# Kernel tuning notes

Hardware: AMD Instinct MI355X
Metric: run time of the kernel (lower is better)

## Reference

```python
import jax, jax.numpy as jnp
import numpy as np

B, D, F_IN, F_OUT = 4, 4096, 128, 128
LEAKY_SLOPE = 0.2


def setup_inputs() -> dict:
    key = jax.random.key(0)
    k_x, k_adj, k_W, k_as, k_at = jax.random.split(key, 5)
    x = jax.random.normal(k_x, (B, D, F_IN), dtype=jnp.float32)
    adj = jax.random.randint(k_adj, (B, D, D), 0, 2, dtype=jnp.int32)
    # xavier-uniform-like init for params
    lim_W = float(np.sqrt(6.0 / (F_IN + F_OUT)))
    W = jax.random.uniform(k_W, (F_IN, F_OUT), minval=-lim_W, maxval=lim_W, dtype=jnp.float32)
    lim_a = float(np.sqrt(6.0 / (F_OUT + 1)))
    a_src = jax.random.uniform(k_as, (F_OUT, 1), minval=-lim_a, maxval=lim_a, dtype=jnp.float32)
    a_tgt = jax.random.uniform(k_at, (F_OUT, 1), minval=-lim_a, maxval=lim_a, dtype=jnp.float32)
    bias = jnp.zeros((F_OUT,), dtype=jnp.float32)
    return {"x": x, "adj": adj, "W": W, "a_src": a_src, "a_tgt": a_tgt, "bias": bias}


def reference(x, adj, W, a_src, a_tgt, bias):
    # x: [B, D, F_in], adj: [B, D, D] (0/1), W: [F_in, F_out]
    Wh = x @ W  # [B, D, F_out]
    f_src = (Wh @ a_src)[..., 0]  # [B, D]
    f_tgt = (Wh @ a_tgt)[..., 0]  # [B, D]
    # additive attention: e_ij = LeakyReLU(f_src_i + f_tgt_j)
    e = jax.nn.leaky_relu(f_src[:, :, None] + f_tgt[:, None, :], negative_slope=LEAKY_SLOPE)  # [B, D, D]
    # torch code masked_fills with -inf then replaces inf with 0 -> masked scores become 0
    e = jnp.where(adj == 0, jnp.zeros((), e.dtype), e)
    attn = jax.nn.softmax(e, axis=-1)  # [B, D, D]
    attn = jnp.clip(attn, 0.0, 1.0)
    h_prime = jnp.einsum('bij,bjf->bif', attn, Wh) + bias  # [B, D, F_out]
    return h_prime, attn
```

## Files before the change

kernel.cpp:

```cpp
#include <hip/hip_runtime.h>

#define BB 4
#define DD 4096
#define FF 128
#define SLOPE 0.2f

typedef float f32x4 __attribute__((ext_vector_type(4)));
typedef int   i32x4 __attribute__((ext_vector_type(4)));
typedef short bf16x8 __attribute__((ext_vector_type(8)));

#define SOFT_BARRIER() do { \
  asm volatile("s_waitcnt lgkmcnt(0)" ::: "memory"); \
  __builtin_amdgcn_s_barrier(); \
} while (0)

__device__ __forceinline__ unsigned short f2bf(float v) {
  union { float f; unsigned u; } c; c.f = v;
  unsigned r = c.u + 0x7FFFu + ((c.u >> 16) & 1u);
  return (unsigned short)(r >> 16);
}

__global__ __launch_bounds__(256) void kA(
    const float* __restrict__ x, const float* __restrict__ W,
    const float* __restrict__ a_src, const float* __restrict__ a_tgt,
    unsigned short* __restrict__ WhT, float* __restrict__ fs,
    float* __restrict__ ft, float* __restrict__ mbpart)
{
  __shared__ __align__(16) float Ws[128 * 128];
  __shared__ __align__(16) float xs[64 * 128];
  __shared__ unsigned short st[128 * 66];
  const int t = threadIdx.x;
  const int wg = blockIdx.x;
  const int row0 = wg * 64;
  const int b = row0 / DD;
  const int i_in_b = row0 % DD;

  for (int i = t * 4; i < 128 * 128; i += 1024)
    *(float4*)&Ws[i] = *(const float4*)&W[i];
  for (int i = t * 4; i < 64 * 128; i += 1024)
    *(float4*)&xs[i] = *(const float4*)&x[(size_t)row0 * FF + i];
  __syncthreads();

  const int fg = t & 31, rg = t >> 5;
  const int f0 = fg * 4, r0 = rg * 8;
  float acc[8][4];
  #pragma unroll
  for (int a = 0; a < 8; ++a) acc[a][0] = acc[a][1] = acc[a][2] = acc[a][3] = 0.f;
  for (int k = 0; k < 128; ++k) {
    float4 wq = *(const float4*)&Ws[k * 128 + f0];
    #pragma unroll
    for (int rr = 0; rr < 8; ++rr) {
      float xv = xs[(r0 + rr) * 128 + k];
      acc[rr][0] += xv * wq.x; acc[rr][1] += xv * wq.y;
      acc[rr][2] += xv * wq.z; acc[rr][3] += xv * wq.w;
    }
  }
  __syncthreads();
  float* red_s = xs;
  float* red_t = xs + 64 * 33;
  float4 as4 = *(const float4*)&a_src[f0];
  float4 at4 = *(const float4*)&a_tgt[f0];
  #pragma unroll
  for (int rr = 0; rr < 8; ++rr) {
    float ps = acc[rr][0]*as4.x + acc[rr][1]*as4.y + acc[rr][2]*as4.z + acc[rr][3]*as4.w;
    float pt = acc[rr][0]*at4.x + acc[rr][1]*at4.y + acc[rr][2]*at4.z + acc[rr][3]*at4.w;
    red_s[(r0 + rr) * 33 + fg] = ps;
    red_t[(r0 + rr) * 33 + fg] = pt;
    st[(f0 + 0) * 66 + r0 + rr] = f2bf(acc[rr][0]);
    st[(f0 + 1) * 66 + r0 + rr] = f2bf(acc[rr][1]);
    st[(f0 + 2) * 66 + r0 + rr] = f2bf(acc[rr][2]);
    st[(f0 + 3) * 66 + r0 + rr] = f2bf(acc[rr][3]);
  }
  __syncthreads();
  if (t < 64) {
    float s = 0.f, tt = 0.f;
    #pragma unroll
    for (int q = 0; q < 32; ++q) { s += red_s[t * 33 + q]; tt += red_t[t * 33 + q]; }
    fs[row0 + t] = s;
    ft[row0 + t] = tt;
    float m = fmaxf(0.f, tt);
    #pragma unroll
    for (int s2 = 1; s2 < 64; s2 <<= 1) m = fmaxf(m, __shfl_xor(m, s2));
    if (t == 0) mbpart[wg] = m;
  }
  for (int p = 0; p < 32; ++p) {
    int idx = p * 256 + t;
    int f = idx >> 6, rl = idx & 63;
    WhT[((size_t)b * FF + f) * DD + i_in_b + rl] = st[f * 66 + rl];
  }
}

__global__ __launch_bounds__(512, 2) void kF(
    const int* __restrict__ adj, const float* __restrict__ fs,
    const float* __restrict__ ft, const float* __restrict__ mbpart,
    const unsigned short* __restrict__ WhT, const float* __restrict__ bias,
    float* __restrict__ hout, float* __restrict__ attn)
{
  __shared__ __align__(16) unsigned short p_lds[2][64 * 256];
  __shared__ __align__(16) unsigned int mlds[64 * 128];
  const int t = threadIdx.x;
  const int w = t >> 6, l = t & 63;
  const int hw = blockIdx.x;
  const int bid = (hw & 7) * 32 + (hw >> 3);
  const int b = bid >> 6;
  const int i0 = (bid & 63) << 6;
  float mbv = mbpart[b * 64 + l];
  #pragma unroll
  for (int s = 1; s < 64; s <<= 1) mbv = fmaxf(mbv, __shfl_xor(mbv, s));
  const int rbase = 8 * w;
  float fsr[8], Mr[8];
  #pragma unroll
  for (int m = 0; m < 8; ++m) {
    fsr[m] = fs[b * DD + i0 + rbase + m];
    Mr[m] = fmaxf(0.f, fsr[m] + mbv);
  }

  const float* ftl = ft + (size_t)b * DD + l * 64;
  float sum[8];
  float inv[8];
  #pragma unroll
  for (int m = 0; m < 8; ++m) sum[m] = 0.f;

  #pragma unroll
  for (int g = 0; g < 2; ++g) {
    const int mb0 = g * 4;
    const int* ap[4];
    #pragma unroll
    for (int m = 0; m < 4; ++m)
      ap[m] = adj + (size_t)(b * DD + i0 + rbase + mb0 + m) * DD + l * 64;
    unsigned lo[4] = {0u, 0u, 0u, 0u}, hi[4] = {0u, 0u, 0u, 0u};

    auto p1_load = [&](i32x4 (&buf)[4][2], int q) {
      #pragma unroll
      for (int m = 0; m < 4; ++m) {
        buf[m][0] = *(const i32x4*)(ap[m] + q * 8);
        buf[m][1] = *(const i32x4*)(ap[m] + q * 8 + 4);
      }
    };
    auto p1_cons = [&](i32x4 (&buf)[4][2], int q) {
      #pragma unroll
      for (int u = 0; u < 2; ++u) {
        const int o = q * 8 + u * 4;
        float4 f = *(const float4*)(ftl + o);
        #pragma unroll
        for (int m = 0; m < 4; ++m) {
          i32x4 a = buf[m][u];
          float e;
          e = fsr[mb0+m] + f.x; e = fmaxf(e, SLOPE * e); e = a.x ? e : 0.f; sum[mb0+m] += __expf(e - Mr[mb0+m]);
          e = fsr[mb0+m] + f.y; e = fmaxf(e, SLOPE * e); e = a.y ? e : 0.f; sum[mb0+m] += __expf(e - Mr[mb0+m]);
          e = fsr[mb0+m] + f.z; e = fmaxf(e, SLOPE * e); e = a.z ? e : 0.f; sum[mb0+m] += __expf(e - Mr[mb0+m]);
          e = fsr[mb0+m] + f.w; e = fmaxf(e, SLOPE * e); e = a.w ? e : 0.f; sum[mb0+m] += __expf(e - Mr[mb0+m]);
          unsigned pack = (a.x ? 1u : 0u) | (a.y ? 2u : 0u) | (a.z ? 4u : 0u) | (a.w ? 8u : 0u);
          if (o < 32) lo[m] |= pack << o; else hi[m] |= pack << (o - 32);
        }
      }
    };

    i32x4 bA[4][2], bB[4][2];
    p1_load(bA, 0);
    p1_load(bB, 1);
    #pragma unroll
    for (int q = 0; q < 8; q += 2) {
      p1_cons(bA, q);
      if (q + 2 < 8) p1_load(bA, q + 2);
      p1_cons(bB, q + 1);
      if (q + 3 < 8) p1_load(bB, q + 3);
    }
    #pragma unroll
    for (int m = 0; m < 4; ++m) {
      uint2 mv; mv.x = lo[m]; mv.y = hi[m];
      *(uint2*)&mlds[(rbase + mb0 + m) * 128 + l * 2] = mv;
    }
  }
  #pragma unroll
  for (int m = 0; m < 8; ++m) {
    #pragma unroll
    for (int s = 1; s < 64; s <<= 1) sum[m] += __shfl_xor(sum[m], s);
    inv[m] = 1.0f / sum[m];
  }

  const float* ftb = ft + (size_t)b * DD;
  float* arow[8];
  unsigned o_[8], wb_[8];
  const int jl = l * 4;
  const unsigned mshift = (unsigned)(jl & 31);
  #pragma unroll
  for (int m = 0; m < 8; ++m) {
    const int r = rbase + m;
    arow[m] = attn + (size_t)b * DD * DD + (size_t)(i0 + r) * DD;
    o_[m] = (((unsigned)r * 512u) + (unsigned)jl * 2u) ^ ((unsigned)(r & 7) << 4);
    wb_[m] = (unsigned)r * 128u + (unsigned)(jl >> 5);
  }
  const int f0 = w * 16;
  const int c15 = l & 15;
  const int kg = l >> 4;
  const unsigned abase = (unsigned)c15 * 512u + (unsigned)kg * 16u;
  const unsigned asw = (unsigned)(c15 & 7) << 4;
  const unsigned short* wrow = WhT + ((size_t)b * FF + f0 + c15) * DD + kg * 8;
  f32x4 acc[4];
  #pragma unroll
  for (int q = 0; q < 4; ++q) acc[q] = (f32x4){0.f, 0.f, 0.f, 0.f};

  bf16x8 BvA[8], BvB[8];
  float4 fA, fB;
  #pragma unroll
  for (int u = 0; u < 8; ++u)
    BvA[u] = *(const bf16x8*)&wrow[(size_t)u * 32];
  fA = *(const float4*)(ftb + jl);

#define CHUNK_BODY(CC, BCUR, BNXT, FCUR, FNXT) do { \
    const int c_ = (CC); \
    const int j_ = c_ * 256 + jl; \
     \
    _Pragma("unroll") \
    for (int u = 0; u < 8; ++u) \
      BNXT[u] = *(const bf16x8*)&wrow[(size_t)((((c_) + 1) & 15) * 8 + u) * 32]; \
    FNXT = *(const float4*)(ftb + ((((c_) + 1) & 15) * 256 + jl)); \
    float4 f4_ = FCUR; \
    f32x4 v_[8]; \
    _Pragma("unroll") \
    for (int m = 0; m < 8; ++m) { \
      unsigned n_ = (mlds[wb_[m] + (unsigned)c_ * 8u] >> mshift) & 0xFu; \
      float e_, p0_, p1_, p2_, p3_; \
      e_ = fsr[m] + f4_.x; e_ = fmaxf(e_, SLOPE * e_); e_ = (n_ & 1u) ? e_ : 0.f; p0_ = __expf(e_ - Mr[m]) * inv[m]; \
      e_ = fsr[m] + f4_.y; e_ = fmaxf(e_, SLOPE * e_); e_ = (n_ & 2u) ? e_ : 0.f; p1_ = __expf(e_ - Mr[m]) * inv[m]; \
      e_ = fsr[m] + f4_.z; e_ = fmaxf(e_, SLOPE * e_); e_ = (n_ & 4u) ? e_ : 0.f; p2_ = __expf(e_ - Mr[m]) * inv[m]; \
      e_ = fsr[m] + f4_.w; e_ = fmaxf(e_, SLOPE * e_); e_ = (n_ & 8u) ? e_ : 0.f; p3_ = __expf(e_ - Mr[m]) * inv[m]; \
      v_[m].x = p0_; v_[m].y = p1_; v_[m].z = p2_; v_[m].w = p3_; \
      ushort4 qv_; qv_.x = f2bf(p0_); qv_.y = f2bf(p1_); qv_.z = f2bf(p2_); qv_.w = f2bf(p3_); \
      *(ushort4*)((char*)&p_lds[c_ & 1][0] + o_[m]) = qv_; \
    } \
    SOFT_BARRIER(); \
     \
    _Pragma("unroll") \
    for (int m = 0; m < 8; ++m) \
      *(f32x4*)(arow[m] + j_) = v_[m]; \
    __builtin_amdgcn_s_setprio(1); \
    _Pragma("unroll") \
    for (int u = 0; u < 8; ++u) { \
      unsigned ao_ = (abase + (unsigned)u * 64u) ^ asw; \
      _Pragma("unroll") \
      for (int T = 0; T < 4; ++T) { \
        bf16x8 A_ = *(const bf16x8*)((const char*)&p_lds[c_ & 1][0] + ao_ + (unsigned)T * 8192u); \
        acc[T] = __builtin_amdgcn_mfma_f32_16x16x32_bf16(A_, BCUR[u], acc[T], 0, 0, 0); \
      } \
    } \
    __builtin_amdgcn_s_setprio(0); \
  } while (0)

  for (int cc = 0; cc < 8; ++cc) {
    CHUNK_BODY(cc * 2,     BvA, BvB, fA, fB);
    CHUNK_BODY(cc * 2 + 1, BvB, BvA, fB, fA);
  }
#undef CHUNK_BODY

  const float bv = bias[f0 + c15];
  #pragma unroll
  for (int T = 0; T < 4; ++T) {
    #pragma unroll
    for (int q = 0; q < 4; ++q) {
      int orow = T * 16 + kg * 4 + q;
      hout[((size_t)b * DD + i0 + orow) * FF + f0 + c15] = acc[T][q] + bv;
    }
  }
}

extern "C" void kernel_launch(void* const* d_in, const int* in_sizes, int n_in,
                              void* d_out, int out_size, void* d_ws, size_t ws_size,
                              hipStream_t stream) {
  const float* x     = (const float*)d_in[0];
  const int*   adj   = (const int*)d_in[1];
  const float* W     = (const float*)d_in[2];
  const float* a_src = (const float*)d_in[3];
  const float* a_tgt = (const float*)d_in[4];
  const float* bias  = (const float*)d_in[5];
  char* ws = (char*)d_ws;
  unsigned short* WhT    = (unsigned short*)ws;
  float*        fs     = (float*)(ws + 4194304);
  float*        ft     = (float*)(ws + 4259840);
  float*        mbpart = (float*)(ws + 4325376);
  float* hout = (float*)d_out;
  float* attn = hout + (size_t)BB * DD * FF;
  kA<<<256, 256, 0, stream>>>(x, W, a_src, a_tgt, WhT, fs, ft, mbpart);
  kF<<<256, 512, 0, stream>>>(adj, fs, ft, mbpart, WhT, bias, hout, attn);
}
```

Baseline: 200.3 us.

## Split softmax row-sum pass into separate kernel and reload adj in main kernel

Moves the first pass (masked exp row sums) out of the fused kernel into a new kernel with one wave per row across many more blocks, writing per-row sums to workspace. The main kernel drops the LDS adjacency bitmask and instead streams adj directly from global memory, prefetching the next chunk per row. The goal is better parallelism for the row-sum pass than 256 large blocks give. In exchange the 256MB adjacency matrix is read twice from HBM, and the main loop now carries global adj loads.

```diff
diff --git a/kernel.cpp b/kernel.cpp
--- a/kernel.cpp
+++ b/kernel.cpp
@@ -90,14 +90,50 @@
   }
 }
 
+__global__ __launch_bounds__(256) void kP1(
+    const int* __restrict__ adj, const float* __restrict__ fs,
+    const float* __restrict__ ft, const float* __restrict__ mbpart,
+    float* __restrict__ sums)
+{
+  const int t = threadIdx.x;
+  const int wv = t >> 6, l = t & 63;
+  const int row = blockIdx.x * 4 + wv;
+  const int b = row >> 12;
+  float mbv = mbpart[b * 64 + l];
+  #pragma unroll
+  for (int s = 1; s < 64; s <<= 1) mbv = fmaxf(mbv, __shfl_xor(mbv, s));
+  const float fsr = fs[row];
+  const float M = fmaxf(0.f, fsr + mbv);
+  const int* arow = adj + (size_t)row * DD + l * 64;
+  const float* ftl = ft + (size_t)b * DD + l * 64;
+  float sum = 0.f;
+  #pragma unroll
+  for (int q = 0; q < 4; ++q) {
+    #pragma unroll
+    for (int u = 0; u < 4; ++u) {
+      const int o = q * 16 + u * 4;
+      i32x4 a = *(const i32x4*)(arow + o);
+      float4 f = *(const float4*)(ftl + o);
+      float e0 = fsr + f.x; e0 = fmaxf(e0, SLOPE * e0); e0 = a.x ? e0 : 0.f;
+      float e1 = fsr + f.y; e1 = fmaxf(e1, SLOPE * e1); e1 = a.y ? e1 : 0.f;
+      float e2 = fsr + f.z; e2 = fmaxf(e2, SLOPE * e2); e2 = a.z ? e2 : 0.f;
+      float e3 = fsr + f.w; e3 = fmaxf(e3, SLOPE * e3); e3 = a.w ? e3 : 0.f;
+      sum += __expf(e0 - M) + __expf(e1 - M) + __expf(e2 - M) + __expf(e3 - M);
+    }
+  }
+  #pragma unroll
+  for (int s = 1; s < 64; s <<= 1) sum += __shfl_xor(sum, s);
+  if (l == 0) sums[row] = sum;
+}
+
 __global__ __launch_bounds__(512, 2) void kF(
     const int* __restrict__ adj, const float* __restrict__ fs,
     const float* __restrict__ ft, const float* __restrict__ mbpart,
-    const unsigned short* __restrict__ WhT, const float* __restrict__ bias,
-    float* __restrict__ hout, float* __restrict__ attn)
+    const float* __restrict__ sums, const unsigned short* __restrict__ WhT,
+    const float* __restrict__ bias, float* __restrict__ hout,
+    float* __restrict__ attn)
 {
   __shared__ __align__(16) unsigned short p_lds[2][64 * 256];
-  __shared__ __align__(16) unsigned int mlds[64 * 128];
   const int t = threadIdx.x;
   const int w = t >> 6, l = t & 63;
   const int hw = blockIdx.x;
@@ -108,88 +144,25 @@
   #pragma unroll
   for (int s = 1; s < 64; s <<= 1) mbv = fmaxf(mbv, __shfl_xor(mbv, s));
   const int rbase = 8 * w;
-  float fsr[8], Mr[8];
+  float fsr[8], Mr[8], inv[8];
   #pragma unroll
   for (int m = 0; m < 8; ++m) {
     fsr[m] = fs[b * DD + i0 + rbase + m];
     Mr[m] = fmaxf(0.f, fsr[m] + mbv);
-  }
-
-  const float* ftl = ft + (size_t)b * DD + l * 64;
-  float sum[8];
-  float inv[8];
-  #pragma unroll
-  for (int m = 0; m < 8; ++m) sum[m] = 0.f;
-
-  #pragma unroll
-  for (int g = 0; g < 2; ++g) {
-    const int mb0 = g * 4;
-    const int* ap[4];
-    #pragma unroll
-    for (int m = 0; m < 4; ++m)
-      ap[m] = adj + (size_t)(b * DD + i0 + rbase + mb0 + m) * DD + l * 64;
-    unsigned lo[4] = {0u, 0u, 0u, 0u}, hi[4] = {0u, 0u, 0u, 0u};
-
-    auto p1_load = [&](i32x4 (&buf)[4][2], int q) {
-      #pragma unroll
-      for (int m = 0; m < 4; ++m) {
-        buf[m][0] = *(const i32x4*)(ap[m] + q * 8);
-        buf[m][1] = *(const i32x4*)(ap[m] + q * 8 + 4);
-      }
-    };
-    auto p1_cons = [&](i32x4 (&buf)[4][2], int q) {
-      #pragma unroll
-      for (int u = 0; u < 2; ++u) {
-        const int o = q * 8 + u * 4;
-        float4 f = *(const float4*)(ftl + o);
-        #pragma unroll
-        for (int m = 0; m < 4; ++m) {
-          i32x4 a = buf[m][u];
-          float e;
-          e = fsr[mb0+m] + f.x; e = fmaxf(e, SLOPE * e); e = a.x ? e : 0.f; sum[mb0+m] += __expf(e - Mr[mb0+m]);
-          e = fsr[mb0+m] + f.y; e = fmaxf(e, SLOPE * e); e = a.y ? e : 0.f; sum[mb0+m] += __expf(e - Mr[mb0+m]);
-          e = fsr[mb0+m] + f.z; e = fmaxf(e, SLOPE * e); e = a.z ? e : 0.f; sum[mb0+m] += __expf(e - Mr[mb0+m]);
-          e = fsr[mb0+m] + f.w; e = fmaxf(e, SLOPE * e); e = a.w ? e : 0.f; sum[mb0+m] += __expf(e - Mr[mb0+m]);
-          unsigned pack = (a.x ? 1u : 0u) | (a.y ? 2u : 0u) | (a.z ? 4u : 0u) | (a.w ? 8u : 0u);
-          if (o < 32) lo[m] |= pack << o; else hi[m] |= pack << (o - 32);
-        }
-      }
-    };
-
-    i32x4 bA[4][2], bB[4][2];
-    p1_load(bA, 0);
-    p1_load(bB, 1);
-    #pragma unroll
-    for (int q = 0; q < 8; q += 2) {
-      p1_cons(bA, q);
-      if (q + 2 < 8) p1_load(bA, q + 2);
-      p1_cons(bB, q + 1);
-      if (q + 3 < 8) p1_load(bB, q + 3);
-    }
-    #pragma unroll
-    for (int m = 0; m < 4; ++m) {
-      uint2 mv; mv.x = lo[m]; mv.y = hi[m];
-      *(uint2*)&mlds[(rbase + mb0 + m) * 128 + l * 2] = mv;
-    }
-  }
-  #pragma unroll
-  for (int m = 0; m < 8; ++m) {
-    #pragma unroll
-    for (int s = 1; s < 64; s <<= 1) sum[m] += __shfl_xor(sum[m], s);
-    inv[m] = 1.0f / sum[m];
+    inv[m] = 1.0f / sums[b * DD + i0 + rbase + m];
   }
 
   const float* ftb = ft + (size_t)b * DD;
+  const int jl = l * 4;
   float* arow[8];
-  unsigned o_[8], wb_[8];
-  const int jl = l * 4;
-  const unsigned mshift = (unsigned)(jl & 31);
+  const int* adjr[8];
+  unsigned o_[8];
   #pragma unroll
   for (int m = 0; m < 8; ++m) {
     const int r = rbase + m;
     arow[m] = attn + (size_t)b * DD * DD + (size_t)(i0 + r) * DD;
+    adjr[m] = adj + (size_t)(b * DD + i0 + r) * DD;
     o_[m] = (((unsigned)r * 512u) + (unsigned)jl * 2u) ^ ((unsigned)(r & 7) << 4);
-    wb_[m] = (unsigned)r * 128u + (unsigned)(jl >> 5);
   }
   const int f0 = w * 16;
   const int c15 = l & 15;
@@ -203,33 +176,42 @@
 
   bf16x8 BvA[8], BvB[8];
   float4 fA, fB;
+  i32x4 adjbuf[8];
   #pragma unroll
   for (int u = 0; u < 8; ++u)
     BvA[u] = *(const bf16x8*)&wrow[(size_t)u * 32];
   fA = *(const float4*)(ftb + jl);
+  #pragma unroll
+  for (int m = 0; m < 8; ++m)
+    adjbuf[m] = *(const i32x4*)(adjr[m] + jl);
 
 #define CHUNK_BODY(CC, BCUR, BNXT, FCUR, FNXT) do { \
     const int c_ = (CC); \
     const int j_ = c_ * 256 + jl; \
+    const int jn_ = (((c_) + 1) & 15) * 256 + jl; \
      \
     _Pragma("unroll") \
     for (int u = 0; u < 8; ++u) \
       BNXT[u] = *(const bf16x8*)&wrow[(size_t)((((c_) + 1) & 15) * 8 + u) * 32]; \
-    FNXT = *(const float4*)(ftb + ((((c_) + 1) & 15) * 256 + jl)); \
+    FNXT = *(const float4*)(ftb + jn_); \
     float4 f4_ = FCUR; \
     f32x4 v_[8]; \
     _Pragma("unroll") \
     for (int m = 0; m < 8; ++m) { \
-      unsigned n_ = (mlds[wb_[m] + (unsigned)c_ * 8u] >> mshift) & 0xFu; \
+      i32x4 a_ = adjbuf[m]; \
       float e_, p0_, p1_, p2_, p3_; \
-      e_ = fsr[m] + f4_.x; e_ = fmaxf(e_, SLOPE * e_); e_ = (n_ & 1u) ? e_ : 0.f; p0_ = __expf(e_ - Mr[m]) * inv[m]; \
-      e_ = fsr[m] + f4_.y; e_ = fmaxf(e_, SLOPE * e_); e_ = (n_ & 2u) ? e_ : 0.f; p1_ = __expf(e_ - Mr[m]) * inv[m]; \
-      e_ = fsr[m] + f4_.z; e_ = fmaxf(e_, SLOPE * e_); e_ = (n_ & 4u) ? e_ : 0.f; p2_ = __expf(e_ - Mr[m]) * inv[m]; \
-      e_ = fsr[m] + f4_.w; e_ = fmaxf(e_, SLOPE * e_); e_ = (n_ & 8u) ? e_ : 0.f; p3_ = __expf(e_ - Mr[m]) * inv[m]; \
+      e_ = fsr[m] + f4_.x; e_ = fmaxf(e_, SLOPE * e_); e_ = a_.x ? e_ : 0.f; p0_ = __expf(e_ - Mr[m]) * inv[m]; \
+      e_ = fsr[m] + f4_.y; e_ = fmaxf(e_, SLOPE * e_); e_ = a_.y ? e_ : 0.f; p1_ = __expf(e_ - Mr[m]) * inv[m]; \
+      e_ = fsr[m] + f4_.z; e_ = fmaxf(e_, SLOPE * e_); e_ = a_.z ? e_ : 0.f; p2_ = __expf(e_ - Mr[m]) * inv[m]; \
+      e_ = fsr[m] + f4_.w; e_ = fmaxf(e_, SLOPE * e_); e_ = a_.w ? e_ : 0.f; p3_ = __expf(e_ - Mr[m]) * inv[m]; \
       v_[m].x = p0_; v_[m].y = p1_; v_[m].z = p2_; v_[m].w = p3_; \
       ushort4 qv_; qv_.x = f2bf(p0_); qv_.y = f2bf(p1_); qv_.z = f2bf(p2_); qv_.w = f2bf(p3_); \
       *(ushort4*)((char*)&p_lds[c_ & 1][0] + o_[m]) = qv_; \
     } \
+     \
+    _Pragma("unroll") \
+    for (int m = 0; m < 8; ++m) \
+      adjbuf[m] = *(const i32x4*)(adjr[m] + jn_); \
     SOFT_BARRIER(); \
      \
     _Pragma("unroll") \
@@ -279,8 +261,10 @@
   float*        fs     = (float*)(ws + 4194304);
   float*        ft     = (float*)(ws + 4259840);
   float*        mbpart = (float*)(ws + 4325376);
+  float*        sums   = (float*)(ws + 4456448);
   float* hout = (float*)d_out;
   float* attn = hout + (size_t)BB * DD * FF;
   kA<<<256, 256, 0, stream>>>(x, W, a_src, a_tgt, WhT, fs, ft, mbpart);
-  kF<<<256, 512, 0, stream>>>(adj, fs, ft, mbpart, WhT, bias, hout, attn);
-}
+  kP1<<<BB * DD / 4, 256, 0, stream>>>(adj, fs, ft, mbpart, sums);
+  kF<<<256, 512, 0, stream>>>(adj, fs, ft, mbpart, sums, WhT, bias, hout, attn);
+}
```

New measurement: 253.1 us. 1.26x slower.
